# Kernel optimization log

Measured on AMD Instinct MI355X. Metric: run time of the kernel, lower is better.

The kernel has to match this reference:

```python
import jax, jax.numpy as jnp
import numpy as np

N_NODES = 100000
N_EDGES = 3200000
IN_FEATS = 512
HIDDEN = 256
N_CLASSES = 64
NITER = 10
HALT_BIAS_INIT = 3.0


def setup_inputs() -> dict:
    key = jax.random.key(0)
    ks = jax.random.split(key, 8)
    x = jax.random.normal(ks[0], (N_NODES, IN_FEATS), dtype=jnp.float32)
    edge_index = jax.random.randint(ks[1], (2, N_EDGES), 0, N_NODES, dtype=jnp.int64)
    # Linear layers: layers[0]: in->hidden, layers[1]: hidden->classes, halt: classes->1
    W0 = jax.random.normal(ks[2], (IN_FEATS, HIDDEN), dtype=jnp.float32) / np.sqrt(IN_FEATS)
    b0 = jnp.zeros((HIDDEN,), dtype=jnp.float32)
    W1 = jax.random.normal(ks[3], (HIDDEN, N_CLASSES), dtype=jnp.float32) / np.sqrt(HIDDEN)
    b1 = jnp.zeros((N_CLASSES,), dtype=jnp.float32)
    Wh = jax.random.normal(ks[4], (N_CLASSES, 1), dtype=jnp.float32) / np.sqrt(N_CLASSES)
    bh = jnp.full((1,), HALT_BIAS_INIT, dtype=jnp.float32)
    return {"x": x, "edge_index": edge_index, "edge_dropout": 0,
            "W0": W0, "b0": b0, "W1": W1, "b1": b1, "Wh": Wh, "bh": bh}


def reference(x, edge_index, edge_dropout, W0, b0, W1, b1, Wh, bh):
    N = x.shape[0]
    # MLP encoder (eval mode: dropout is identity)
    h = jax.nn.relu(x @ W0 + b0)
    h = h @ W1 + b1                                   # [N, C]

    # gcn_norm with self-loops (edge_dropout=0 in eval => identical every iter)
    loops = jnp.arange(N, dtype=edge_index.dtype)
    row = jnp.concatenate([edge_index[0], loops])     # source
    col = jnp.concatenate([edge_index[1], loops])     # target (aggregation index)
    deg = jax.ops.segment_sum(jnp.ones_like(col, dtype=h.dtype), col, num_segments=N)
    dinv = jnp.where(deg > 0, deg ** -0.5, 0.0)
    norm = dinv[row] * dinv[col]                      # [E+N]

    def step(ph, _):
        msg = norm[:, None] * ph[row]                 # gather + scale, [E+N, C]
        ph2 = jax.ops.segment_sum(msg, col, num_segments=N)  # scatter_add
        logit = jnp.clip(ph2 @ Wh + bh, -10.0, 10.0)  # [N, 1]
        return ph2, (ph2, logit)

    _, (props, logits) = jax.lax.scan(step, h, None, length=NITER)
    outputs = jnp.concatenate([h[None], props], axis=0)       # [niter+1, N, C]
    halting_logits = jnp.transpose(logits[:, :, 0])           # [N, niter]

    lam = jax.nn.sigmoid(halting_logits)
    remain = jnp.cumprod(1.0 - lam, axis=1)                   # inclusive
    remain_excl = jnp.concatenate([jnp.ones((N, 1), lam.dtype), remain[:, :-1]], axis=1)
    p = lam * remain_excl
    p = p.at[:, -1].add(remain[:, -1])                        # leftover mass to last step
    return outputs, p, halting_logits
```

## Files before the change

### kernel.cpp

```cpp
#include <hip/hip_runtime.h>
#include <hip/hip_bf16.h>

#define N_NODES  100000
#define N_EDGES  3200000
#define IN_FEATS 512
#define HIDDEN   256
#define N_CLASSES 64
#define NITER    10

#define SCAN_NB  49
#define FCH      4096
#define NCHUNKF  ((N_EDGES + FCH - 1) / FCH)

#define OUT_P_OFF  ((size_t)(NITER + 1) * N_NODES * N_CLASSES)
#define OUT_HL_OFF (OUT_P_OFF + (size_t)N_NODES * NITER)

#define WS_META_INTS (4 * N_NODES + 128)
#define WS_CSR_OFF   ((size_t)WS_META_INTS * 4)
#define WS_W0F_OFF   (WS_CSR_OFF + (size_t)2 * N_EDGES * 4)
#define WS_W1F_OFF   (WS_W0F_OFF + 262144)
#define WS_SH0_OFF   (WS_W1F_OFF + 32768)
#define WS_SH1_OFF   (WS_SH0_OFF + (size_t)N_NODES * 64 * 2)
#define WS_NEED_W    (WS_SH0_OFF)
#define WS_NEED_BF   (WS_SH1_OFF + (size_t)N_NODES * 64 * 2)

typedef _Float16 f16x8 __attribute__((ext_vector_type(8)));
typedef _Float16 f16x4 __attribute__((ext_vector_type(4)));
typedef float    f32x4 __attribute__((ext_vector_type(4)));

__device__ __forceinline__ float bflo(unsigned v) { return __uint_as_float(v << 16); }
__device__ __forceinline__ float bfhi(unsigned v) { return __uint_as_float(v & 0xffff0000u); }
__device__ __forceinline__ unsigned short f2bf(float f) {
    unsigned u = __float_as_uint(f);
    return (unsigned short)((u + 0x7fffu + ((u >> 16) & 1u)) >> 16);
}

__global__ void k_detect(const int* ei, int* flag) {
    if (threadIdx.x == 0 && blockIdx.x == 0) {
        int is64 = 1;
        for (int k = 0; k < 128; ++k) {
            if (ei[2 * k + 1] != 0) { is64 = 0; break; }
        }
        *flag = is64;
    }
}

__device__ __forceinline__ int edge_row_nt(const void* ei, int is64, int e) {
    return is64 ? (int)__builtin_nontemporal_load((const long long*)ei + e)
                : __builtin_nontemporal_load((const int*)ei + e);
}
__device__ __forceinline__ int edge_col_nt(const void* ei, int is64, int e) {
    return is64 ? (int)__builtin_nontemporal_load((const long long*)ei + (size_t)N_EDGES + e)
                : __builtin_nontemporal_load((const int*)ei + (size_t)N_EDGES + e);
}

__global__ void k_count(const void* ei, const int* flag, int* cnt) {
    int e = blockIdx.x * 256 + threadIdx.x;
    if (e >= N_EDGES) return;
    int is64 = *flag;
    atomicAdd(&cnt[edge_col_nt(ei, is64, e)], 1);
}

__global__ __launch_bounds__(256) void k_scan1(const int* cnt, int* part) {
    __shared__ int sd[256];
    int b = blockIdx.x, t = threadIdx.x;
    int s = 0;
    for (int j = t; j < 2048; j += 256) {
        int idx = b * 2048 + j;
        if (idx < N_NODES) s += cnt[idx];
    }
    sd[t] = s;
    __syncthreads();
    for (int o = 128; o > 0; o >>= 1) {
        if (t < o) sd[t] += sd[t + o];
        __syncthreads();
    }
    if (t == 0) part[b] = sd[0];
}

__global__ __launch_bounds__(256) void k_scan2(int* part, int* offs) {
    __shared__ int sd[256];
    int t = threadIdx.x;
    sd[t] = (t < SCAN_NB) ? part[t] : 0;
    __syncthreads();
    for (int o = 1; o < 256; o <<= 1) {
        int add = (t >= o) ? sd[t - o] : 0;
        __syncthreads();
        sd[t] += add;
        __syncthreads();
    }
    if (t < SCAN_NB) part[t] = (t == 0) ? 0 : sd[t - 1];
    if (t == 0) offs[N_NODES] = N_EDGES;
}

__global__ __launch_bounds__(256) void k_scan3(const int* cnt, const int* part, int* offs) {
    __shared__ int sd[256];
    int b = blockIdx.x, t = threadIdx.x;
    int base = b * 2048 + t * 8;
    int local[8];
    int s = 0;
#pragma unroll
    for (int j = 0; j < 8; ++j) {
        int idx = base + j;
        int v = (idx < N_NODES) ? cnt[idx] : 0;
        local[j] = s;
        s += v;
    }
    sd[t] = s;
    __syncthreads();
    for (int o = 1; o < 256; o <<= 1) {
        int add = (t >= o) ? sd[t - o] : 0;
        __syncthreads();
        sd[t] += add;
        __syncthreads();
    }
    int tbase = part[b] + ((t == 0) ? 0 : sd[t - 1]);
#pragma unroll
    for (int j = 0; j < 8; ++j) {
        int idx = base + j;
        if (idx < N_NODES) offs[idx] = tbase + local[j];
    }
}

__global__ void k_dinv(const int* cnt, float* dinv) {
    int i = blockIdx.x * 256 + threadIdx.x;
    if (i >= N_NODES) return;
    dinv[i] = rsqrtf((float)(cnt[i] + 1));
}

__global__ __launch_bounds__(256) void k_fill_x(const void* ei, const int* flag,
        const int* offs, int* cursor, int* csr, int* tick) {
    __shared__ int sxcc, schunk;
    if (threadIdx.x == 0) {
        int x;
        asm volatile("s_getreg_b32 %0, hwreg(HW_REG_XCC_ID)" : "=s"(x));
        sxcc = x & 7;
    }
    __syncthreads();
    const int g = sxcc;
    const int lo = g * (N_NODES / 8);
    const int hi = lo + (N_NODES / 8);
    const int is64 = *flag;
    for (;;) {
        __syncthreads();
        if (threadIdx.x == 0) schunk = atomicAdd(&tick[g * 8], 1);
        __syncthreads();
        int ch = schunk;
        if (ch >= NCHUNKF) break;
        int e0 = ch * FCH;
        int e1 = e0 + FCH; if (e1 > N_EDGES) e1 = N_EDGES;
        for (int e = e0 + threadIdx.x; e < e1; e += 256) {
            int c = edge_col_nt(ei, is64, e);
            if (c >= lo && c < hi) {
                int r = edge_row_nt(ei, is64, e);
                int pos = offs[c] + atomicAdd(&cursor[c], 1);
                csr[pos] = r << 7;
            }
        }
    }
}

__global__ void k_prep_w(const float* __restrict__ W0, const float* __restrict__ W1,
                         _Float16* __restrict__ W0f, _Float16* __restrict__ W1f) {
    int id = blockIdx.x * 256 + threadIdx.x;
    if (id < 16384) {
        int l = id & 63, c = (id >> 6) & 15, kkg = id >> 10;
        int n = c * 16 + (l & 15);
        int kb = kkg * 32 + ((l >> 4) * 8);
        f16x8 v;
#pragma unroll
        for (int j = 0; j < 8; ++j) v[j] = (_Float16)W0[(size_t)(kb + j) * HIDDEN + n];
        *(f16x8*)&W0f[(size_t)id * 8] = v;
    } else if (id < 16384 + 2048) {
        int id2 = id - 16384;
        int l = id2 & 63, c = (id2 >> 6) & 3, kkg = id2 >> 8;
        int n = c * 16 + (l & 15);
        int kb = kkg * 32 + ((l >> 4) * 8);
        f16x8 v;
#pragma unroll
        for (int j = 0; j < 8; ++j) v[j] = (_Float16)W1[(size_t)(kb + j) * N_CLASSES + n];
        *(f16x8*)&W1f[(size_t)id2 * 8] = v;
    }
}

#define EBM 64
#define XS_STRIDE 72
#define H1_STRIDE 264
#define XS0   0
#define XS1   9216
#define WST0  18432
#define WST1  34816
#define W2ST0 34816
#define W2ST1 38912
__global__ __launch_bounds__(256) void k_encoder_mfma(
        const float* __restrict__ x, const _Float16* __restrict__ W0f,
        const float* __restrict__ b0, const _Float16* __restrict__ W1f,
        const float* __restrict__ b1, float* __restrict__ out,
        const float* __restrict__ dinv,
        unsigned short* __restrict__ shadow, int write_shadow) {
    __shared__ char smem[51200];
    const int t = threadIdx.x;
    const int w = t >> 6, l = t & 63;
    const int g = l >> 4, r15 = l & 15;
    const int row0 = blockIdx.x * EBM;
    const int c4 = t & 15;
    const int srow0 = t >> 4;

    f32x4 acc[16];
#pragma unroll
    for (int c = 0; c < 16; ++c) acc[c] = (f32x4){0.f, 0.f, 0.f, 0.f};

    float4 xld[4];
    f16x8 wld[4];
#pragma unroll
    for (int q = 0; q < 4; ++q) {
        int grow = row0 + q * 16 + srow0;
        if (grow >= N_NODES) grow = N_NODES - 1;
        xld[q] = *(const float4*)&x[(size_t)grow * IN_FEATS + c4 * 4];
    }
#pragma unroll
    for (int q = 0; q < 4; ++q) wld[q] = *(const f16x8*)&W0f[(size_t)(q * 256 + t) * 8];
#pragma unroll
    for (int q = 0; q < 4; ++q) {
        f16x4 hv = {(_Float16)xld[q].x, (_Float16)xld[q].y, (_Float16)xld[q].z, (_Float16)xld[q].w};
        *(f16x4*)(smem + XS0 + ((q * 16 + srow0) * XS_STRIDE + c4 * 4) * 2) = hv;
    }
#pragma unroll
    for (int q = 0; q < 4; ++q)
        *(f16x8*)(smem + WST0 + (q * 256 + t) * 16) = wld[q];
    __syncthreads();

    for (int kkg = 0; kkg < 16; ++kkg) {
        const int kc = kkg >> 1, kk = kkg & 1;
        if (kkg < 15) {
#pragma unroll
            for (int q = 0; q < 4; ++q)
                wld[q] = *(const f16x8*)&W0f[(size_t)((kkg + 1) * 1024 + q * 256 + t) * 8];
        }
        if (kk == 0 && kc < 7) {
#pragma unroll
            for (int q = 0; q < 4; ++q) {
                int grow = row0 + q * 16 + srow0;
                if (grow >= N_NODES) grow = N_NODES - 1;
                xld[q] = *(const float4*)&x[(size_t)grow * IN_FEATS + (kc + 1) * 64 + c4 * 4];
            }
        }
        const char* xbase = smem + ((kc & 1) ? XS1 : XS0);
        const char* wbase = smem + ((kkg & 1) ? WST1 : WST0);
        f16x8 af = *(const f16x8*)(xbase + ((w * 16 + r15) * XS_STRIDE + kk * 32 + g * 8) * 2);
#pragma unroll
        for (int c = 0; c < 16; ++c) {
            f16x8 bf = *(const f16x8*)(wbase + ((c << 6) | l) * 16);
            acc[c] = __builtin_amdgcn_mfma_f32_16x16x32_f16(af, bf, acc[c], 0, 0, 0);
        }
        if (kkg < 15) {
            char* wdst = smem + ((kkg & 1) ? WST0 : WST1);
#pragma unroll
            for (int q = 0; q < 4; ++q)
                *(f16x8*)(wdst + (q * 256 + t) * 16) = wld[q];
        }
        if (kk == 1 && kc < 7) {
            char* xdst = smem + ((kc & 1) ? XS0 : XS1);
#pragma unroll
            for (int q = 0; q < 4; ++q) {
                f16x4 hv = {(_Float16)xld[q].x, (_Float16)xld[q].y, (_Float16)xld[q].z, (_Float16)xld[q].w};
                *(f16x4*)(xdst + ((q * 16 + srow0) * XS_STRIDE + c4 * 4) * 2) = hv;
            }
        }
        __syncthreads();
    }

    f16x8 w2ld = *(const f16x8*)&W1f[(size_t)t * 8];
#pragma unroll
    for (int c = 0; c < 16; ++c) {
        float bb = b0[c * 16 + r15];
#pragma unroll
        for (int i = 0; i < 4; ++i) {
            int row = w * 16 + g * 4 + i;
            *(_Float16*)(smem + (row * H1_STRIDE + c * 16 + r15) * 2) =
                (_Float16)fmaxf(acc[c][i] + bb, 0.f);
        }
    }
    *(f16x8*)(smem + W2ST0 + t * 16) = w2ld;
    __syncthreads();

    f32x4 acc2[4];
#pragma unroll
    for (int c = 0; c < 4; ++c) acc2[c] = (f32x4){0.f, 0.f, 0.f, 0.f};
    for (int kkg = 0; kkg < 8; ++kkg) {
        if (kkg < 7) w2ld = *(const f16x8*)&W1f[(size_t)((kkg + 1) * 256 + t) * 8];
        const char* wbase = smem + ((kkg & 1) ? W2ST1 : W2ST0);
        f16x8 af = *(const f16x8*)(smem + ((w * 16 + r15) * H1_STRIDE + kkg * 32 + g * 8) * 2);
#pragma unroll
        for (int c = 0; c < 4; ++c) {
            f16x8 bf = *(const f16x8*)(wbase + ((c << 6) | l) * 16);
            acc2[c] = __builtin_amdgcn_mfma_f32_16x16x32_f16(af, bf, acc2[c], 0, 0, 0);
        }
        if (kkg < 7)
            *(f16x8*)(smem + ((kkg & 1) ? W2ST0 : W2ST1) + t * 16) = w2ld;
        __syncthreads();
    }
#pragma unroll
    for (int c = 0; c < 4; ++c) {
        float bb = b1[c * 16 + r15];
#pragma unroll
        for (int i = 0; i < 4; ++i) {
            int row = row0 + w * 16 + g * 4 + i;
            if (row < N_NODES) {
                float v = acc2[c][i] + bb;
                int col = c * 16 + r15;
                out[(size_t)row * 64 + col] = v;
                if (write_shadow)
                    shadow[(size_t)row * 64 + col] = f2bf(dinv[row] * v);
            }
        }
    }
}

__global__ __launch_bounds__(256) void k_encoder(const float* __restrict__ x,
        const float* __restrict__ W0, const float* __restrict__ b0,
        const float* __restrict__ W1, const float* __restrict__ b1,
        float* __restrict__ out) {
    __shared__ float xsh[32][128];
    __shared__ float h1s[32][HIDDEN + 1];
    const int t = threadIdx.x;
    const int rg = t >> 6;
    const int cg = t & 63;
    const size_t row0 = (size_t)blockIdx.x * 32;
    float acc[8][4];
#pragma unroll
    for (int i = 0; i < 8; ++i)
        acc[i][0] = acc[i][1] = acc[i][2] = acc[i][3] = 0.f;
    for (int kc = 0; kc < 4; ++kc) {
        __syncthreads();
#pragma unroll
        for (int q = 0; q < 4; ++q) {
            int idx = t + q * 256;
            int r = idx >> 5, pos = idx & 31;
            *(float4*)&xsh[r][pos * 4] =
                *(const float4*)&x[(row0 + r) * IN_FEATS + kc * 128 + pos * 4];
        }
        __syncthreads();
        for (int kk = 0; kk < 128; kk += 4) {
            float4 xv[8];
#pragma unroll
            for (int i = 0; i < 8; ++i) xv[i] = *(const float4*)&xsh[rg * 8 + i][kk];
#pragma unroll
            for (int j = 0; j < 4; ++j) {
                float4 wv = *(const float4*)&W0[(size_t)(kc * 128 + kk + j) * HIDDEN + cg * 4];
#pragma unroll
                for (int i = 0; i < 8; ++i) {
                    float xj = (&xv[i].x)[j];
                    acc[i][0] = fmaf(xj, wv.x, acc[i][0]);
                    acc[i][1] = fmaf(xj, wv.y, acc[i][1]);
                    acc[i][2] = fmaf(xj, wv.z, acc[i][2]);
                    acc[i][3] = fmaf(xj, wv.w, acc[i][3]);
                }
            }
        }
    }
    float4 bb = *(const float4*)&b0[cg * 4];
#pragma unroll
    for (int i = 0; i < 8; ++i) {
        int r = rg * 8 + i;
        h1s[r][cg * 4 + 0] = fmaxf(acc[i][0] + bb.x, 0.f);
        h1s[r][cg * 4 + 1] = fmaxf(acc[i][1] + bb.y, 0.f);
        h1s[r][cg * 4 + 2] = fmaxf(acc[i][2] + bb.z, 0.f);
        h1s[r][cg * 4 + 3] = fmaxf(acc[i][3] + bb.w, 0.f);
    }
    __syncthreads();
    float a2[8];
#pragma unroll
    for (int i = 0; i < 8; ++i) a2[i] = 0.f;
    for (int k = 0; k < HIDDEN; ++k) {
        float wv = W1[(size_t)k * N_CLASSES + cg];
#pragma unroll
        for (int i = 0; i < 8; ++i) a2[i] = fmaf(h1s[rg * 8 + i][k], wv, a2[i]);
    }
    float bv = b1[cg];
#pragma unroll
    for (int i = 0; i < 8; ++i)
        out[(row0 + rg * 8 + i) * N_CLASSES + cg] = a2[i] + bv;
}

__global__ __launch_bounds__(256) void k_prop_s(
        const unsigned short* __restrict__ pin_s, float* __restrict__ pout,
        unsigned short* __restrict__ pout_s, const int* __restrict__ offs,
        const int* __restrict__ csr, const float* __restrict__ dinv,
        const float* __restrict__ Wh, const float* __restrict__ bh,
        float* __restrict__ hl, int t) {
    int node = (blockIdx.x * 256 + threadIdx.x) >> 5;
    if (node >= N_NODES) return;
    int hlane = threadIdx.x & 31;
    int base = threadIdx.x & 32;
    const char* gbase = (const char*)pin_s + hlane * 4;
    unsigned own = *(const unsigned*)(gbase + ((size_t)node << 7));
    float a0 = bflo(own), a1 = bfhi(own);
    float c0 = 0.f, c1 = 0.f;
    int e0 = offs[node], e1 = offs[node + 1];
    for (int eb = e0; eb < e1; eb += 32) {
        int n = e1 - eb; if (n > 32) n = 32;
        int idx = eb + hlane;
        int ew = csr[idx < e1 ? idx : e1 - 1];
        int j = 0;
        for (; j + 16 <= n; j += 16) {
            unsigned v[16];
#pragma unroll
            for (int q = 0; q < 16; ++q) {
                int s = __shfl(ew, base + j + q, 64);
                v[q] = *(const unsigned*)(gbase + s);
            }
#pragma unroll
            for (int q = 0; q < 16; ++q) {
                if (q & 1) { c0 += bflo(v[q]); c1 += bfhi(v[q]); }
                else       { a0 += bflo(v[q]); a1 += bfhi(v[q]); }
            }
        }
        for (; j + 8 <= n; j += 8) {
            unsigned v[8];
#pragma unroll
            for (int q = 0; q < 8; ++q) {
                int s = __shfl(ew, base + j + q, 64);
                v[q] = *(const unsigned*)(gbase + s);
            }
#pragma unroll
            for (int q = 0; q < 8; ++q) {
                if (q & 1) { c0 += bflo(v[q]); c1 += bfhi(v[q]); }
                else       { a0 += bflo(v[q]); a1 += bfhi(v[q]); }
            }
        }
        for (; j < n; ++j) {
            int s = __shfl(ew, base + j, 64);
            unsigned v = *(const unsigned*)(gbase + s);
            a0 += bflo(v);
            a1 += bfhi(v);
        }
    }
    float di = dinv[node];
    float fa = di * (a0 + c0), fb = di * (a1 + c1);
    *(float2*)&pout[(size_t)node * 64 + hlane * 2] = make_float2(fa, fb);
    *(unsigned*)&pout_s[(size_t)node * 64 + hlane * 2] =
        (unsigned)f2bf(di * fa) | ((unsigned)f2bf(di * fb) << 16);
    float2 wh = *(const float2*)&Wh[hlane * 2];
    float s = fa * wh.x + fb * wh.y;
#pragma unroll
    for (int o = 16; o > 0; o >>= 1) s += __shfl_xor(s, o, 64);
    if (hlane == 0) {
        float lg = s + bh[0];
        lg = fminf(10.0f, fmaxf(-10.0f, lg));
        hl[(size_t)node * NITER + t] = lg;
    }
}

__global__ __launch_bounds__(256) void k_prop(const float* __restrict__ pin,
        float* __restrict__ pout, const int* __restrict__ offs,
        const int* __restrict__ csr, const float* __restrict__ dinv,
        const float* __restrict__ Wh, const float* __restrict__ bh,
        float* __restrict__ hl, int t) {
    int wid = (blockIdx.x * blockDim.x + threadIdx.x) >> 6;
    int lane = threadIdx.x & 63;
    if (wid >= N_NODES) return;
    float di = dinv[wid];
    float a[4];
    a[0] = di * di * pin[(size_t)wid * 64 + lane];
    a[1] = a[2] = a[3] = 0.f;
    int e0 = offs[wid], e1 = offs[wid + 1];
    for (int eb = e0; eb < e1; eb += 64) {
        int n = e1 - eb; if (n > 64) n = 64;
        int idx = eb + lane;
        int ew = csr[idx < e1 ? idx : e1 - 1];
        int j = 0;
        for (; j + 8 <= n; j += 8) {
            float v[8], w[8];
#pragma unroll
            for (int q = 0; q < 8; ++q) {
                int r = __shfl(ew, j + q, 64) >> 7;
                w[q] = dinv[r] * di;
                v[q] = pin[(size_t)r * 64 + lane];
            }
#pragma unroll
            for (int q = 0; q < 8; ++q) a[q & 3] = fmaf(w[q], v[q], a[q & 3]);
        }
        for (; j < n; ++j) {
            int r = __shfl(ew, j, 64) >> 7;
            a[0] = fmaf(dinv[r] * di, pin[(size_t)r * 64 + lane], a[0]);
        }
    }
    float acc = (a[0] + a[1]) + (a[2] + a[3]);
    pout[(size_t)wid * 64 + lane] = acc;
    float s = acc * Wh[lane];
#pragma unroll
    for (int o = 32; o > 0; o >>= 1) s += __shfl_xor(s, o, 64);
    if (lane == 0) {
        float lg = s + bh[0];
        lg = fminf(10.0f, fmaxf(-10.0f, lg));
        hl[(size_t)wid * NITER + t] = lg;
    }
}

__global__ void k_p(const float* __restrict__ hl, float* __restrict__ p) {
    int i = blockIdx.x * 256 + threadIdx.x;
    if (i >= N_NODES) return;
    float remain = 1.0f;
    float pv[NITER];
#pragma unroll
    for (int t = 0; t < NITER; ++t) {
        float lg = hl[(size_t)i * NITER + t];
        float lam = 1.0f / (1.0f + expf(-lg));
        pv[t] = lam * remain;
        remain *= (1.0f - lam);
    }
    pv[NITER - 1] += remain;
#pragma unroll
    for (int t = 0; t < NITER; ++t) p[(size_t)i * NITER + t] = pv[t];
}

extern "C" void kernel_launch(void* const* d_in, const int* in_sizes, int n_in,
                              void* d_out, int out_size, void* d_ws, size_t ws_size,
                              hipStream_t stream) {
    const float* x  = (const float*)d_in[0];
    const void*  ei = d_in[1];
    const float* W0 = (const float*)d_in[3];
    const float* b0 = (const float*)d_in[4];
    const float* W1 = (const float*)d_in[5];
    const float* b1 = (const float*)d_in[6];
    const float* Wh = (const float*)d_in[7];
    const float* bh = (const float*)d_in[8];
    float* out = (float*)d_out;

    int* ws_i   = (int*)d_ws;
    int* cnt    = ws_i;
    int* offs   = ws_i + N_NODES;
    int* cursor = ws_i + 2 * N_NODES + 2;
    int* part   = ws_i + 3 * N_NODES + 2;
    int* flag   = ws_i + 3 * N_NODES + 66;
    int* tick   = ws_i + 3 * N_NODES + 70;
    float* dinv = (float*)(ws_i + 3 * N_NODES + 128);
    int* csr    = (int*)((char*)d_ws + WS_CSR_OFF);
    _Float16* W0f = (_Float16*)((char*)d_ws + WS_W0F_OFF);
    _Float16* W1f = (_Float16*)((char*)d_ws + WS_W1F_OFF);
    unsigned short* sh0 = (unsigned short*)((char*)d_ws + WS_SH0_OFF);
    unsigned short* sh1 = (unsigned short*)((char*)d_ws + WS_SH1_OFF);

    const int use_w  = ws_size >= WS_NEED_W;
    const int use_bf = ws_size >= WS_NEED_BF;

    hipMemsetAsync(d_ws, 0, (size_t)(3 * N_NODES + 128) * 4, stream);
    k_detect<<<1, 64, 0, stream>>>((const int*)ei, flag);
    k_count<<<(N_EDGES + 255) / 256, 256, 0, stream>>>(ei, flag, cnt);
    k_scan1<<<SCAN_NB, 256, 0, stream>>>(cnt, part);
    k_scan2<<<1, 256, 0, stream>>>(part, offs);
    k_scan3<<<SCAN_NB, 256, 0, stream>>>(cnt, part, offs);
    k_dinv<<<(N_NODES + 255) / 256, 256, 0, stream>>>(cnt, dinv);
    k_fill_x<<<2048, 256, 0, stream>>>(ei, flag, offs, cursor, csr, tick);

    if (use_w) {
        k_prep_w<<<72, 256, 0, stream>>>(W0, W1, W0f, W1f);
        k_encoder_mfma<<<(N_NODES + EBM - 1) / EBM, 256, 0, stream>>>(
            x, W0f, b0, W1f, b1, out, dinv, sh0, use_bf);
    } else {
        k_encoder<<<N_NODES / 32, 256, 0, stream>>>(x, W0, b0, W1, b1, out);
    }

    float* hl = out + OUT_HL_OFF;
    if (use_bf) {
        for (int it = 0; it < NITER; ++it) {
            const unsigned short* pin_s = (it & 1) ? sh1 : sh0;
            unsigned short* pout_s      = (it & 1) ? sh0 : sh1;
            float* pout = out + (size_t)(it + 1) * N_NODES * N_CLASSES;
            k_prop_s<<<((size_t)N_NODES * 32 + 255) / 256, 256, 0, stream>>>(
                pin_s, pout, pout_s, offs, csr, dinv, Wh, bh, hl, it);
        }
    } else {
        for (int it = 0; it < NITER; ++it) {
            const float* pin = out + (size_t)it * N_NODES * N_CLASSES;
            float* pout      = out + (size_t)(it + 1) * N_NODES * N_CLASSES;
            k_prop<<<((size_t)N_NODES * 64 + 255) / 256, 256, 0, stream>>>(
                pin, pout, offs, csr, dinv, Wh, bh, hl, it);
        }
    }
    k_p<<<(N_NODES + 255) / 256, 256, 0, stream>>>(hl, out + OUT_P_OFF);
}
```

Baseline: 1.015 ms.

## Build CSR via rank capture and XCD-bucketed binning instead of cursor atomics

The count pass now records each edge's rank within its target node. A bucketing pass writes (position, row) pairs into eight node-range bins, and a per-XCD pass scatters them into the CSR. This replaces the fill kernel, which reread all edges on every XCD and used per-node cursor atomics, with one edge read plus a partitioned scatter. The cost is extra workspace, an extra rank16 write and read, and a staged bin buffer. The rank is stored as 16 bits, so the result is wrong for any node with in-degree above 65535.

```diff
diff --git a/kernel.cpp b/kernel.cpp
--- a/kernel.cpp
+++ b/kernel.cpp
@@ -9,6 +9,7 @@
 #define NITER    10
 
 #define SCAN_NB  49
+#define NPB      12500
 #define FCH      4096
 #define NCHUNKF  ((N_EDGES + FCH - 1) / FCH)
 
@@ -17,12 +18,15 @@
 
 #define WS_META_INTS (4 * N_NODES + 128)
 #define WS_CSR_OFF   ((size_t)WS_META_INTS * 4)
+#define WS_RANK_OFF  (WS_CSR_OFF + (size_t)N_EDGES * 4)
 #define WS_W0F_OFF   (WS_CSR_OFF + (size_t)2 * N_EDGES * 4)
 #define WS_W1F_OFF   (WS_W0F_OFF + 262144)
 #define WS_SH0_OFF   (WS_W1F_OFF + 32768)
 #define WS_SH1_OFF   (WS_SH0_OFF + (size_t)N_NODES * 64 * 2)
+#define WS_BIN_OFF   (WS_SH1_OFF + (size_t)N_NODES * 64 * 2)
 #define WS_NEED_W    (WS_SH0_OFF)
-#define WS_NEED_BF   (WS_SH1_OFF + (size_t)N_NODES * 64 * 2)
+#define WS_NEED_BF   (WS_BIN_OFF)
+#define WS_NEED_BIN  (WS_BIN_OFF + (size_t)N_EDGES * 8)
 
 typedef _Float16 f16x8 __attribute__((ext_vector_type(8)));
 typedef _Float16 f16x4 __attribute__((ext_vector_type(4)));
@@ -45,6 +49,13 @@
     }
 }
 
+__device__ __forceinline__ int edge_row(const void* ei, int is64, int e) {
+    return is64 ? (int)((const long long*)ei)[e] : ((const int*)ei)[e];
+}
+__device__ __forceinline__ int edge_col(const void* ei, int is64, int e) {
+    return is64 ? (int)((const long long*)ei)[(size_t)N_EDGES + e]
+                : ((const int*)ei)[(size_t)N_EDGES + e];
+}
 __device__ __forceinline__ int edge_row_nt(const void* ei, int is64, int e) {
     return is64 ? (int)__builtin_nontemporal_load((const long long*)ei + e)
                 : __builtin_nontemporal_load((const int*)ei + e);
@@ -54,11 +65,13 @@
                 : __builtin_nontemporal_load((const int*)ei + (size_t)N_EDGES + e);
 }
 
-__global__ void k_count(const void* ei, const int* flag, int* cnt) {
+__global__ void k_count_rank(const void* ei, const int* flag, int* cnt,
+                             unsigned short* rank16) {
     int e = blockIdx.x * 256 + threadIdx.x;
     if (e >= N_EDGES) return;
     int is64 = *flag;
-    atomicAdd(&cnt[edge_col_nt(ei, is64, e)], 1);
+    int rank = atomicAdd(&cnt[edge_col_nt(ei, is64, e)], 1);
+    rank16[e] = (unsigned short)rank;
 }
 
 __global__ __launch_bounds__(256) void k_scan1(const int* cnt, int* part) {
@@ -128,6 +141,56 @@
     dinv[i] = rsqrtf((float)(cnt[i] + 1));
 }
 
+__global__ __launch_bounds__(256) void k_bucket(const void* ei, const int* flag,
+        const unsigned short* __restrict__ rank16, const int* __restrict__ offs,
+        int* bcur, uint2* __restrict__ bin) {
+    __shared__ int lcnt[8], gbase[8];
+    if (threadIdx.x < 8) lcnt[threadIdx.x] = 0;
+    __syncthreads();
+    int e = blockIdx.x * 256 + threadIdx.x;
+    int is64 = *flag;
+    int c = edge_col_nt(ei, is64, e);
+    int r = edge_row_nt(ei, is64, e);
+    unsigned b = (unsigned)c / (unsigned)NPB;
+    int lp = atomicAdd(&lcnt[b], 1);
+    __syncthreads();
+    if (threadIdx.x < 8) {
+        int n = lcnt[threadIdx.x];
+        gbase[threadIdx.x] = n ? atomicAdd(&bcur[threadIdx.x * 8], n) : 0;
+    }
+    __syncthreads();
+    int pos = offs[c] + rank16[e];
+    int dst = offs[b * NPB] + gbase[b] + lp;
+    bin[dst] = make_uint2((unsigned)pos, (unsigned)(r << 7));
+}
+
+__global__ __launch_bounds__(256) void k_csr(const uint2* __restrict__ bin,
+        const int* __restrict__ offs, int* __restrict__ csr, int* tick) {
+    __shared__ int sxcc, schunk;
+    if (threadIdx.x == 0) {
+        int x;
+        asm volatile("s_getreg_b32 %0, hwreg(HW_REG_XCC_ID)" : "=s"(x));
+        sxcc = x & 7;
+    }
+    __syncthreads();
+    const int g = sxcc;
+    const int base = offs[g * NPB];
+    const int end  = (g == 7) ? N_EDGES : offs[(g + 1) * NPB];
+    const int size = end - base;
+    for (;;) {
+        __syncthreads();
+        if (threadIdx.x == 0) schunk = atomicAdd(&tick[g * 8], 1);
+        __syncthreads();
+        int i0 = schunk * FCH;
+        if (i0 >= size) break;
+        int i1 = i0 + FCH; if (i1 > size) i1 = size;
+        for (int i = i0 + threadIdx.x; i < i1; i += 256) {
+            uint2 pe = bin[base + i];
+            csr[pe.x] = (int)pe.y;
+        }
+    }
+}
+
 __global__ __launch_bounds__(256) void k_fill_x(const void* ei, const int* flag,
         const int* offs, int* cursor, int* csr, int* tick) {
     __shared__ int sxcc, schunk;
@@ -138,8 +201,8 @@
     }
     __syncthreads();
     const int g = sxcc;
-    const int lo = g * (N_NODES / 8);
-    const int hi = lo + (N_NODES / 8);
+    const int lo = g * NPB;
+    const int hi = lo + NPB;
     const int is64 = *flag;
     for (;;) {
         __syncthreads();
@@ -532,27 +595,36 @@
     int* cnt    = ws_i;
     int* offs   = ws_i + N_NODES;
     int* cursor = ws_i + 2 * N_NODES + 2;
+    int* bcur   = cursor;
     int* part   = ws_i + 3 * N_NODES + 2;
     int* flag   = ws_i + 3 * N_NODES + 66;
     int* tick   = ws_i + 3 * N_NODES + 70;
     float* dinv = (float*)(ws_i + 3 * N_NODES + 128);
     int* csr    = (int*)((char*)d_ws + WS_CSR_OFF);
+    unsigned short* rank16 = (unsigned short*)((char*)d_ws + WS_RANK_OFF);
     _Float16* W0f = (_Float16*)((char*)d_ws + WS_W0F_OFF);
     _Float16* W1f = (_Float16*)((char*)d_ws + WS_W1F_OFF);
     unsigned short* sh0 = (unsigned short*)((char*)d_ws + WS_SH0_OFF);
     unsigned short* sh1 = (unsigned short*)((char*)d_ws + WS_SH1_OFF);
-
-    const int use_w  = ws_size >= WS_NEED_W;
-    const int use_bf = ws_size >= WS_NEED_BF;
+    uint2* bin = (uint2*)((char*)d_ws + WS_BIN_OFF);
+
+    const int use_w   = ws_size >= WS_NEED_W;
+    const int use_bf  = ws_size >= WS_NEED_BF;
+    const int use_bin = ws_size >= WS_NEED_BIN;
 
     hipMemsetAsync(d_ws, 0, (size_t)(3 * N_NODES + 128) * 4, stream);
     k_detect<<<1, 64, 0, stream>>>((const int*)ei, flag);
-    k_count<<<(N_EDGES + 255) / 256, 256, 0, stream>>>(ei, flag, cnt);
+    k_count_rank<<<(N_EDGES + 255) / 256, 256, 0, stream>>>(ei, flag, cnt, rank16);
     k_scan1<<<SCAN_NB, 256, 0, stream>>>(cnt, part);
     k_scan2<<<1, 256, 0, stream>>>(part, offs);
     k_scan3<<<SCAN_NB, 256, 0, stream>>>(cnt, part, offs);
     k_dinv<<<(N_NODES + 255) / 256, 256, 0, stream>>>(cnt, dinv);
-    k_fill_x<<<2048, 256, 0, stream>>>(ei, flag, offs, cursor, csr, tick);
+    if (use_bin) {
+        k_bucket<<<N_EDGES / 256, 256, 0, stream>>>(ei, flag, rank16, offs, bcur, bin);
+        k_csr<<<2048, 256, 0, stream>>>(bin, offs, csr, tick);
+    } else {
+        k_fill_x<<<2048, 256, 0, stream>>>(ei, flag, offs, cursor, csr, tick);
+    }
 
     if (use_w) {
         k_prep_w<<<72, 256, 0, stream>>>(W0, W1, W0f, W1f);
```

Result: slower. 1.109 ms (+9.3%).
